# Performance work log

Measured on AMD Instinct MI355X. Metric: run time of the kernel, lower is better.

The kernel has to match this reference:

```python
import jax, jax.numpy as jnp
import numpy as np

B, N, IN_F = 16, 1024, 256
HEADS, OUT_F = 4, 64
NEG_SLOPE = 0.2
CLAMP_MIN = -1e9
MASK_VAL = -9e15


def setup_inputs() -> dict:
    key = jax.random.key(0)
    k1, k2, k3, k4 = jax.random.split(key, 4)
    x = jax.random.normal(k1, (B, N, IN_F), dtype=jnp.float32)
    adj = jax.random.randint(k2, (B, N, N), 0, 2, dtype=jnp.int32)
    # Linear weight, stored as (in, heads*out) so y = x @ W (xavier-uniform scale)
    lim_w = float(np.sqrt(6.0 / (IN_F + HEADS * OUT_F)))
    W = jax.random.uniform(k3, (IN_F, HEADS * OUT_F), dtype=jnp.float32,
                           minval=-lim_w, maxval=lim_w)
    lim_a = float(np.sqrt(6.0 / (2 * OUT_F + HEADS)))
    a = jax.random.uniform(k4, (2 * OUT_F, HEADS), dtype=jnp.float32,
                           minval=-lim_a, maxval=lim_a)
    return {"x": x, "adj": adj, "W": W, "a": a}


def reference(x, adj, W, a):
    Bs, Ns, _ = x.shape
    # Projection: (B,N,H,D)
    h = (x @ W).reshape(Bs, Ns, HEADS, OUT_F)
    # cat([h_i, h_j]) . a == h_i . a_src + h_j . a_dst  (exact same math, no O(N^2*2D) tensor)
    a_src, a_dst = a[:OUT_F], a[OUT_F:]          # each (D, H)
    s_src = jnp.einsum('bnhd,dh->bnh', h, a_src)  # score contribution of node i
    s_dst = jnp.einsum('bnhd,dh->bnh', h, a_dst)  # score contribution of node j
    e = jax.nn.leaky_relu(s_src[:, :, None, :] + s_dst[:, None, :, :],
                          negative_slope=NEG_SLOPE)  # (B,N,N,H)
    # match original: subtract unmasked row max, clamp, then mask, then softmax over j
    e = e - jnp.max(e, axis=2, keepdims=True)
    e = jnp.maximum(e, CLAMP_MIN)
    att = jnp.where(adj[..., None] > 0, e, MASK_VAL)
    att = jax.nn.softmax(att, axis=2)
    h_prime = jnp.einsum('bijh,bjhd->bihd', att, h)  # (B,N,H,D)
    return h_prime.reshape(Bs, Ns, HEADS * OUT_F)
```

## Files before the change

kernel.cpp:

```cpp
#include <hip/hip_runtime.h>
#include <hip/hip_bf16.h>

#define B_   16
#define N_   1024
#define INF_ 256
#define NH_  4
#define HD_  256
#define L2E  1.4426950408889634f

typedef __attribute__((ext_vector_type(8))) short short8;
typedef __attribute__((ext_vector_type(4))) float f32x4;

__device__ __forceinline__ float bf2f(unsigned short u) {
    union { unsigned int i; float f; } v; v.i = ((unsigned int)u) << 16; return v.f;
}
__device__ __forceinline__ unsigned short f2bf(float f) {
    union { float f; unsigned int i; } v; v.f = f;
    unsigned int x = v.i;
    return (unsigned short)((x + 0x7fffu + ((x >> 16) & 1u)) >> 16);
}
__device__ __forceinline__ unsigned int cvt_pk_bf16(float lo, float hi) {
    unsigned int r;
    asm("v_cvt_pk_bf16_f32 %0, %1, %2" : "=v"(r) : "v"(lo), "v"(hi));
    return r;
}

__global__ __launch_bounds__(256) void k_prep(const int* __restrict__ adj,
                                              const float* __restrict__ W,
                                              unsigned int* __restrict__ pb,
                                              unsigned short* __restrict__ wswz)
{
    int bx = blockIdx.x, t = threadIdx.x;
    if (bx < 2048) {
        int wave = t >> 6, lane = t & 63;
        int row = bx * 8 + wave * 2 + (lane >> 5);
        int w   = lane & 31;
        const int4* ar = (const int4*)(adj + ((long)row << 10) + w * 32);
        unsigned int u = 0;
        #pragma unroll
        for (int k = 0; k < 8; k++) {
            int4 a = ar[k];
            u |= ((unsigned)a.x) << (4 * k);
            u |= ((unsigned)a.y) << (4 * k + 1);
            u |= ((unsigned)a.z) << (4 * k + 2);
            u |= ((unsigned)a.w) << (4 * k + 3);
        }
        pb[((long)w << 14) + row] = u;
    } else {
        int slot = (bx - 2048) * 256 + t;
        int kstep = slot >> 10;
        int nt    = (slot >> 6) & 15;
        int lane  = slot & 63;
        int k0 = kstep * 32 + (lane >> 4) * 8;
        int n  = nt * 16 + (lane & 15);
        ushort4 o0, o1;
        o0.x = f2bf(W[(k0 + 0) * HD_ + n]);
        o0.y = f2bf(W[(k0 + 1) * HD_ + n]);
        o0.z = f2bf(W[(k0 + 2) * HD_ + n]);
        o0.w = f2bf(W[(k0 + 3) * HD_ + n]);
        o1.x = f2bf(W[(k0 + 4) * HD_ + n]);
        o1.y = f2bf(W[(k0 + 5) * HD_ + n]);
        o1.z = f2bf(W[(k0 + 6) * HD_ + n]);
        o1.w = f2bf(W[(k0 + 7) * HD_ + n]);
        *(ushort4*)&wswz[(long)slot * 8]     = o0;
        *(ushort4*)&wswz[(long)slot * 8 + 4] = o1;
    }
}

__global__ __launch_bounds__(256) void k_gemm_h(
    const float* __restrict__ x, const float* __restrict__ a,
    const unsigned short* __restrict__ wswz,
    unsigned short* __restrict__ hswz,
    float* __restrict__ esr, float2* __restrict__ edst)
{
    __shared__ unsigned short xls[16][264];
    int t = threadIdx.x;
    int blk = blockIdx.x;
    int row0 = blk * 16;
    int b  = blk >> 6;
    int n0 = row0 & 1023;

    {
        int sr = t >> 4, sc = (t & 15) * 16;
        const float* xp = x + (long)(row0 + sr) * INF_ + sc;
        float4 v0 = ((const float4*)xp)[0];
        float4 v1 = ((const float4*)xp)[1];
        float4 v2 = ((const float4*)xp)[2];
        float4 v3 = ((const float4*)xp)[3];
        ushort4 u0 = {f2bf(v0.x), f2bf(v0.y), f2bf(v0.z), f2bf(v0.w)};
        ushort4 u1 = {f2bf(v1.x), f2bf(v1.y), f2bf(v1.z), f2bf(v1.w)};
        ushort4 u2 = {f2bf(v2.x), f2bf(v2.y), f2bf(v2.z), f2bf(v2.w)};
        ushort4 u3 = {f2bf(v3.x), f2bf(v3.y), f2bf(v3.z), f2bf(v3.w)};
        *(ushort4*)&xls[sr][sc]      = u0;
        *(ushort4*)&xls[sr][sc + 4]  = u1;
        *(ushort4*)&xls[sr][sc + 8]  = u2;
        *(ushort4*)&xls[sr][sc + 12] = u3;
    }
    __syncthreads();

    int wave = t >> 6, lane = t & 63, quad = lane >> 4, l15 = lane & 15;
    f32x4 acc[4];
    #pragma unroll
    for (int i = 0; i < 4; i++) acc[i] = (f32x4){0.f, 0.f, 0.f, 0.f};

    #pragma unroll
    for (int ks = 0; ks < 8; ks++) {
        short8 af = *(const short8*)&xls[l15][ks * 32 + quad * 8];
        #pragma unroll
        for (int nt = 0; nt < 4; nt++) {
            short8 bf = *(const short8*)(wswz +
                ((long)((ks * 16 + wave * 4 + nt) * 64 + lane)) * 8);
            acc[nt] = __builtin_amdgcn_mfma_f32_16x16x32_bf16(af, bf, acc[nt], 0, 0, 0);
        }
    }

    int q0 = (quad & 1) * 4;
    int qd = ((row0 & 31) + quad * 4) >> 3;
    long bj32 = row0 >> 5;
    #pragma unroll
    for (int nt = 0; nt < 4; nt++) {
        int dg = wave * 4 + nt;
        long idx8 = (bj32 * 16 + dg) * 64 + qd * 16 + l15;
        ushort4 o = {f2bf(acc[nt][0]), f2bf(acc[nt][1]),
                     f2bf(acc[nt][2]), f2bf(acc[nt][3])};
        *(ushort4*)&hswz[idx8 * 8 + q0] = o;
    }

    float as_[4], ad_[4];
    #pragma unroll
    for (int nt = 0; nt < 4; nt++) {
        int d = nt * 16 + l15;
        as_[nt] = a[d * NH_ + wave];
        ad_[nt] = a[(64 + d) * NH_ + wave];
    }
    #pragma unroll
    for (int r = 0; r < 4; r++) {
        float ps = acc[0][r] * as_[0] + acc[1][r] * as_[1]
                 + acc[2][r] * as_[2] + acc[3][r] * as_[3];
        float pd = acc[0][r] * ad_[0] + acc[1][r] * ad_[1]
                 + acc[2][r] * ad_[2] + acc[3][r] * ad_[3];
        #pragma unroll
        for (int m = 1; m < 16; m <<= 1) {
            ps += __shfl_xor(ps, m);
            pd += __shfl_xor(pd, m);
        }
        if (l15 == 0) {
            int row = n0 + quad * 4 + r;
            float s1 = ps * L2E, s2 = pd * L2E;
            esr[((long)b * NH_ + wave) * N_ + row] = __builtin_exp2f(-0.8f * s1);
            edst[((long)b * NH_ + wave) * N_ + row] =
                make_float2(__builtin_exp2f(s2), __builtin_exp2f(0.2f * s2));
        }
    }
}

__global__ __launch_bounds__(1024, 4) void k_attn(
    const unsigned int* __restrict__ pb, const unsigned short* __restrict__ hswz,
    const float* __restrict__ esr, const float2* __restrict__ edst,
    float* __restrict__ out)
{
    __shared__ float2 esb[1024];
    __shared__ uint2 mtab[16];

    int t = threadIdx.x;
    int bid = blockIdx.x;
    int swz = (bid & 7) * 32 + (bid >> 3);
    int b  = swz >> 4;
    int hh = (swz >> 2) & 3;
    int rg = swz & 3;
    int row0 = rg * 256;

    int wave = t >> 6, lane = t & 63, quad = lane >> 4, l15 = lane & 15;

    esb[t] = edst[((long)(b * NH_ + hh)) * N_ + t];
    if (t < 16) {
        int k = t;
        unsigned int w0 = ((k & 1) ? 0xffffu : 0u) | ((k & 2) ? 0xffff0000u : 0u);
        unsigned int w1 = ((k & 4) ? 0xffffu : 0u) | ((k & 8) ? 0xffff0000u : 0u);
        mtab[k] = make_uint2(w0, w1);
    }
    __syncthreads();

    int irow = row0 + wave * 16 + l15;
    float r0 = esr[((long)(b * NH_ + hh)) * N_ + irow];
    const unsigned int* pbw = pb + ((long)b << 10) + irow;

    f32x4 acc[4], dn;
    #pragma unroll
    for (int i = 0; i < 4; i++) acc[i] = (f32x4){0.f, 0.f, 0.f, 0.f};
    dn = (f32x4){0.f, 0.f, 0.f, 0.f};
    short8 ones;
    #pragma unroll
    for (int i = 0; i < 8; i++) ones[i] = (short)0x3F80;

    int shq = quad * 8;

    #pragma unroll 4
    for (int jc = 0; jc < 32; jc++) {
        unsigned int m0 = (pbw[((long)jc << 14)] >> shq) & 0xffu;
        const f32x4* ej = (const f32x4*)&esb[jc * 32 + quad * 8];

        union { unsigned int u[4]; short8 s; } p0;
        #pragma unroll
        for (int qp = 0; qp < 4; qp++) {
            f32x4 d = ej[qp];
            p0.u[qp] = cvt_pk_bf16(fmaxf(d[0], r0 * d[1]), fmaxf(d[2], r0 * d[3]));
        }
        uint2 ma = mtab[m0 & 15u], mb = mtab[m0 >> 4];
        p0.u[0] &= ma.x; p0.u[1] &= ma.y; p0.u[2] &= mb.x; p0.u[3] &= mb.y;

        long s8 = ((long)(b * 32 + jc)) * 1024;
        #pragma unroll
        for (int idt = 0; idt < 4; idt++) {
            short8 bf = *(const short8*)(hswz + (s8 + (hh * 4 + idt) * 64 + lane) * 8);
            acc[idt] = __builtin_amdgcn_mfma_f32_16x16x32_bf16(p0.s, bf, acc[idt], 0, 0, 0);
        }
        dn = __builtin_amdgcn_mfma_f32_16x16x32_bf16(p0.s, ones, dn, 0, 0, 0);
    }

    float inv[4];
    #pragma unroll
    for (int r = 0; r < 4; r++) inv[r] = 1.0f / dn[r];
    #pragma unroll
    for (int idt = 0; idt < 4; idt++) {
        int col = hh * 64 + idt * 16 + l15;
        #pragma unroll
        for (int r = 0; r < 4; r++) {
            long row_g = (long)b * N_ + row0 + wave * 16 + quad * 4 + r;
            out[row_g * HD_ + col] = acc[idt][r] * inv[r];
        }
    }
}

extern "C" void kernel_launch(void* const* d_in, const int* in_sizes, int n_in,
                              void* d_out, int out_size, void* d_ws, size_t ws_size,
                              hipStream_t stream) {
    const float* x   = (const float*)d_in[0];
    const int*   adj = (const int*)d_in[1];
    const float* W   = (const float*)d_in[2];
    const float* a   = (const float*)d_in[3];
    float* out = (float*)d_out;

    unsigned int* pb      = (unsigned int*)d_ws;
    unsigned short* hswz  = (unsigned short*)(pb + 524288);
    unsigned short* wswz  = hswz + (long)B_ * N_ * HD_;
    float* esr   = (float*)(wswz + INF_ * HD_);
    float2* edst = (float2*)(esr + (long)B_ * NH_ * N_);

    k_prep<<<2080, 256, 0, stream>>>(adj, W, pb, wswz);
    k_gemm_h<<<1024, 256, 0, stream>>>(x, a, wswz, hswz, esr, edst);
    k_attn<<<256, 1024, 0, stream>>>(pb, hswz, esr, edst, out);
}
```

Measured before the change: 149.5 us.

## Enlarge projection GEMM tile to 64 rows to reuse W fragments

```diff
diff --git a/kernel.cpp b/kernel.cpp
--- a/kernel.cpp
+++ b/kernel.cpp
@@ -67,63 +67,79 @@
     }
 }
 
-__global__ __launch_bounds__(256) void k_gemm_h(
+__global__ __launch_bounds__(256, 4) void k_gemm_h(
     const float* __restrict__ x, const float* __restrict__ a,
     const unsigned short* __restrict__ wswz,
     unsigned short* __restrict__ hswz,
     float* __restrict__ esr, float2* __restrict__ edst)
 {
-    __shared__ unsigned short xls[16][264];
+    __shared__ unsigned short xls[64][264];
     int t = threadIdx.x;
     int blk = blockIdx.x;
-    int row0 = blk * 16;
-    int b  = blk >> 6;
+    int row0 = blk * 64;
+    int b  = blk >> 4;
     int n0 = row0 & 1023;
 
     {
-        int sr = t >> 4, sc = (t & 15) * 16;
-        const float* xp = x + (long)(row0 + sr) * INF_ + sc;
-        float4 v0 = ((const float4*)xp)[0];
-        float4 v1 = ((const float4*)xp)[1];
-        float4 v2 = ((const float4*)xp)[2];
-        float4 v3 = ((const float4*)xp)[3];
-        ushort4 u0 = {f2bf(v0.x), f2bf(v0.y), f2bf(v0.z), f2bf(v0.w)};
-        ushort4 u1 = {f2bf(v1.x), f2bf(v1.y), f2bf(v1.z), f2bf(v1.w)};
-        ushort4 u2 = {f2bf(v2.x), f2bf(v2.y), f2bf(v2.z), f2bf(v2.w)};
-        ushort4 u3 = {f2bf(v3.x), f2bf(v3.y), f2bf(v3.z), f2bf(v3.w)};
-        *(ushort4*)&xls[sr][sc]      = u0;
-        *(ushort4*)&xls[sr][sc + 4]  = u1;
-        *(ushort4*)&xls[sr][sc + 8]  = u2;
-        *(ushort4*)&xls[sr][sc + 12] = u3;
+        int sr0 = t >> 4, sc = (t & 15) * 16;
+        #pragma unroll
+        for (int rr = 0; rr < 4; rr++) {
+            int sr = sr0 + rr * 16;
+            const float* xp = x + (long)(row0 + sr) * INF_ + sc;
+            float4 v0 = ((const float4*)xp)[0];
+            float4 v1 = ((const float4*)xp)[1];
+            float4 v2 = ((const float4*)xp)[2];
+            float4 v3 = ((const float4*)xp)[3];
+            ushort4 u0 = {f2bf(v0.x), f2bf(v0.y), f2bf(v0.z), f2bf(v0.w)};
+            ushort4 u1 = {f2bf(v1.x), f2bf(v1.y), f2bf(v1.z), f2bf(v1.w)};
+            ushort4 u2 = {f2bf(v2.x), f2bf(v2.y), f2bf(v2.z), f2bf(v2.w)};
+            ushort4 u3 = {f2bf(v3.x), f2bf(v3.y), f2bf(v3.z), f2bf(v3.w)};
+            *(ushort4*)&xls[sr][sc]      = u0;
+            *(ushort4*)&xls[sr][sc + 4]  = u1;
+            *(ushort4*)&xls[sr][sc + 8]  = u2;
+            *(ushort4*)&xls[sr][sc + 12] = u3;
+        }
     }
     __syncthreads();
 
     int wave = t >> 6, lane = t & 63, quad = lane >> 4, l15 = lane & 15;
-    f32x4 acc[4];
-    #pragma unroll
-    for (int i = 0; i < 4; i++) acc[i] = (f32x4){0.f, 0.f, 0.f, 0.f};
+    f32x4 acc[4][4];
+    #pragma unroll
+    for (int rg = 0; rg < 4; rg++)
+        #pragma unroll
+        for (int nt = 0; nt < 4; nt++) acc[rg][nt] = (f32x4){0.f, 0.f, 0.f, 0.f};
 
     #pragma unroll
     for (int ks = 0; ks < 8; ks++) {
-        short8 af = *(const short8*)&xls[l15][ks * 32 + quad * 8];
+        short8 bfr[4];
+        #pragma unroll
+        for (int nt = 0; nt < 4; nt++)
+            bfr[nt] = *(const short8*)(wswz +
+                ((long)((ks * 16 + wave * 4 + nt) * 64 + lane)) * 8);
+        #pragma unroll
+        for (int rg = 0; rg < 4; rg++) {
+            short8 af = *(const short8*)&xls[rg * 16 + l15][ks * 32 + quad * 8];
+            #pragma unroll
+            for (int nt = 0; nt < 4; nt++)
+                acc[rg][nt] = __builtin_amdgcn_mfma_f32_16x16x32_bf16(
+                    af, bfr[nt], acc[rg][nt], 0, 0, 0);
+        }
+    }
+
+    int q0 = (quad & 1) * 4;
+    #pragma unroll
+    for (int rg = 0; rg < 4; rg++) {
+        int row0g = row0 + rg * 16;
+        int qd = ((row0g & 31) + quad * 4) >> 3;
+        long bj32 = row0g >> 5;
         #pragma unroll
         for (int nt = 0; nt < 4; nt++) {
-            short8 bf = *(const short8*)(wswz +
-                ((long)((ks * 16 + wave * 4 + nt) * 64 + lane)) * 8);
-            acc[nt] = __builtin_amdgcn_mfma_f32_16x16x32_bf16(af, bf, acc[nt], 0, 0, 0);
-        }
-    }
-
-    int q0 = (quad & 1) * 4;
-    int qd = ((row0 & 31) + quad * 4) >> 3;
-    long bj32 = row0 >> 5;
-    #pragma unroll
-    for (int nt = 0; nt < 4; nt++) {
-        int dg = wave * 4 + nt;
-        long idx8 = (bj32 * 16 + dg) * 64 + qd * 16 + l15;
-        ushort4 o = {f2bf(acc[nt][0]), f2bf(acc[nt][1]),
-                     f2bf(acc[nt][2]), f2bf(acc[nt][3])};
-        *(ushort4*)&hswz[idx8 * 8 + q0] = o;
+            int dg = wave * 4 + nt;
+            long idx8 = (bj32 * 16 + dg) * 64 + qd * 16 + l15;
+            ushort4 o = {f2bf(acc[rg][nt][0]), f2bf(acc[rg][nt][1]),
+                         f2bf(acc[rg][nt][2]), f2bf(acc[rg][nt][3])};
+            *(ushort4*)&hswz[idx8 * 8 + q0] = o;
+        }
     }
 
     float as_[4], ad_[4];
@@ -134,22 +150,25 @@
         ad_[nt] = a[(64 + d) * NH_ + wave];
     }
     #pragma unroll
-    for (int r = 0; r < 4; r++) {
-        float ps = acc[0][r] * as_[0] + acc[1][r] * as_[1]
-                 + acc[2][r] * as_[2] + acc[3][r] * as_[3];
-        float pd = acc[0][r] * ad_[0] + acc[1][r] * ad_[1]
-                 + acc[2][r] * ad_[2] + acc[3][r] * ad_[3];
-        #pragma unroll
-        for (int m = 1; m < 16; m <<= 1) {
-            ps += __shfl_xor(ps, m);
-            pd += __shfl_xor(pd, m);
-        }
-        if (l15 == 0) {
-            int row = n0 + quad * 4 + r;
-            float s1 = ps * L2E, s2 = pd * L2E;
-            esr[((long)b * NH_ + wave) * N_ + row] = __builtin_exp2f(-0.8f * s1);
-            edst[((long)b * NH_ + wave) * N_ + row] =
-                make_float2(__builtin_exp2f(s2), __builtin_exp2f(0.2f * s2));
+    for (int rg = 0; rg < 4; rg++) {
+        #pragma unroll
+        for (int r = 0; r < 4; r++) {
+            float ps = acc[rg][0][r] * as_[0] + acc[rg][1][r] * as_[1]
+                     + acc[rg][2][r] * as_[2] + acc[rg][3][r] * as_[3];
+            float pd = acc[rg][0][r] * ad_[0] + acc[rg][1][r] * ad_[1]
+                     + acc[rg][2][r] * ad_[2] + acc[rg][3][r] * ad_[3];
+            #pragma unroll
+            for (int m = 1; m < 16; m <<= 1) {
+                ps += __shfl_xor(ps, m);
+                pd += __shfl_xor(pd, m);
+            }
+            if (l15 == 0) {
+                int row = n0 + rg * 16 + quad * 4 + r;
+                float s1 = ps * L2E, s2 = pd * L2E;
+                esr[((long)b * NH_ + wave) * N_ + row] = __builtin_exp2f(-0.8f * s1);
+                edst[((long)b * NH_ + wave) * N_ + row] =
+                    make_float2(__builtin_exp2f(s2), __builtin_exp2f(0.2f * s2));
+            }
         }
     }
 }
@@ -195,7 +214,7 @@
 
     int shq = quad * 8;
 
-    #pragma unroll 4
+    #pragma unroll 8
     for (int jc = 0; jc < 32; jc++) {
         unsigned int m0 = (pbw[((long)jc << 14)] >> shq) & 0xffu;
         const f32x4* ej = (const f32x4*)&esb[jc * 32 + quad * 8];
@@ -248,6 +267,6 @@
     float2* edst = (float2*)(esr + (long)B_ * NH_ * N_);
 
     k_prep<<<2080, 256, 0, stream>>>(adj, W, pb, wswz);
-    k_gemm_h<<<1024, 256, 0, stream>>>(x, a, wswz, hswz, esr, edst);
+    k_gemm_h<<<256, 256, 0, stream>>>(x, a, wswz, hswz, esr, edst);
     k_attn<<<256, 1024, 0, stream>>>(pb, hswz, esr, edst, out);
 }
```

Result: no change. 149.3 us (-0.1%).
